# Performance work log

Hardware: AMD Instinct MI355X
Metric: run time of the kernel (lower is better)

The kernel has to match this reference:

```python
import jax, jax.numpy as jnp
import numpy as np

B, N, ND, ED, H, E = 4, 512, 2, 1, 32, 32  # batch, nodes, node_dim, edge_dim, latent, enc


def _xavier(key, shape):
    fan_in, fan_out = shape
    s = jnp.sqrt(2.0 / (fan_in + fan_out)).astype(jnp.float32)
    return jax.random.normal(key, shape, dtype=jnp.float32) * s


def setup_inputs() -> dict:
    key = jax.random.key(0)
    ks = jax.random.split(key, 12)
    return {
        "x": jax.random.normal(ks[0], (B, N, ND), dtype=jnp.float32),
        "h": jax.random.normal(ks[1], (B, N, H), dtype=jnp.float32),
        "adj": jax.random.randint(ks[2], (B, N, N), 0, 2, dtype=jnp.int64) if jax.config.jax_enable_x64 else jax.random.randint(ks[2], (B, N, N), 0, 2, dtype=jnp.int32),
        "e_feat": jax.random.uniform(ks[3], (B, N, N, ED), dtype=jnp.float32),
        "W_ne": _xavier(ks[4], (ND + H, E)), "b_ne": jnp.zeros((E,), jnp.float32),
        "W_ee": _xavier(ks[5], (ED, E)), "b_ee": jnp.zeros((E,), jnp.float32),
        "W_m": _xavier(ks[6], (2 * E + E, H)), "b_m": jnp.zeros((H,), jnp.float32),
        "W_u": _xavier(ks[7], (E + H, H)), "b_u": jnp.zeros((H,), jnp.float32),
        "W_dec": _xavier(ks[8], (H + E, ND)), "b_dec": jnp.zeros((ND,), jnp.float32),
        "W_p": _xavier(ks[9], (2 * H + E, 1)), "b_p": jnp.zeros((1,), jnp.float32),
        "W_t": _xavier(ks[10], (H, 1)), "b_t": jnp.zeros((1,), jnp.float32),
    }


def reference(x, h, adj, e_feat, W_ne, b_ne, W_ee, b_ee, W_m, b_m, W_u, b_u,
              W_dec, b_dec, W_p, b_p, W_t, b_t):
    b, n = x.shape[0], x.shape[1]
    # add self-loops (adj = adj + I), then boolean mask
    mask = (adj + jnp.eye(n, dtype=adj.dtype)[None]) > 0  # [B,N,N]

    # node encoder: z = Linear([x, h])
    z = jnp.concatenate([x, h], axis=-1) @ W_ne + b_ne  # [B,N,E]
    # edge encoder
    e = e_feat @ W_ee + b_ee  # [B,N,N,E]

    # MPNN processor: pairwise messages m_ij = ReLU(M([z_i, z_j, e_ij]))
    zi = jnp.broadcast_to(z[:, :, None, :], (b, n, n, z.shape[-1]))
    zj = jnp.broadcast_to(z[:, None, :, :], (b, n, n, z.shape[-1]))
    m = jax.nn.relu(jnp.concatenate([zi, zj, e], axis=-1) @ W_m + b_m)  # [B,N,N,H]
    m = jnp.where(mask[..., None], m, -1e9)
    agg = jnp.max(m, axis=2)  # max over senders j -> [B,N,H]
    new_h = jax.nn.relu(jnp.concatenate([z, agg], axis=-1) @ W_u + b_u)  # [B,N,H]

    # decoder and termination head
    new_x = jnp.concatenate([z, new_h], axis=-1) @ W_dec + b_dec  # [B,N,ND]
    tau = jnp.mean(new_h, axis=1) @ W_t + b_t  # [B,1]

    # predecessor head (pred=1): pairwise scores masked with -inf off-graph
    hi = jnp.broadcast_to(new_h[:, :, None, :], (b, n, n, new_h.shape[-1]))
    hj = jnp.broadcast_to(new_h[:, None, :, :], (b, n, n, new_h.shape[-1]))
    p = (jnp.concatenate([hi, hj, e], axis=-1) @ W_p + b_p)[..., 0]  # [B,N,N]
    p = jnp.where(mask, p, -jnp.inf)

    return new_x, p, tau, new_h
```

## Files before the change

kernel.cpp:

```cpp
#include <hip/hip_runtime.h>
#include <math.h>

#define BQ 4
#define NQ 512
#define NDQ 2

#define NEG_BIG (-1.0e30f)

__device__ __forceinline__ float4 fmax4(float4 a, float4 b) {
    return make_float4(fmaxf(a.x, b.x), fmaxf(a.y, b.y), fmaxf(a.z, b.z), fmaxf(a.w, b.w));
}
__device__ __forceinline__ void upd(float4& m, float e, float4 ck, float4 bv) {
    m.x = fmaxf(m.x, fmaf(e, ck.x, bv.x));
    m.y = fmaxf(m.y, fmaf(e, ck.y, bv.y));
    m.z = fmaxf(m.z, fmaf(e, ck.z, bv.z));
    m.w = fmaxf(m.w, fmaf(e, ck.w, bv.w));
}

__global__ __launch_bounds__(256) void k_encode(
    const float* __restrict__ x, const float* __restrict__ h,
    const float* __restrict__ W_ne, const float* __restrict__ b_ne,
    const float* __restrict__ W_m,
    const float* __restrict__ W_ee, const float* __restrict__ b_ee,
    const float* __restrict__ b_m,
    const float* __restrict__ W_p, const float* __restrict__ b_p,
    float* __restrict__ ws_z, float* __restrict__ ws_bv,
    float* __restrict__ ws_c, float* __restrict__ ws_d,
    float* __restrict__ ws_c2d2, float* __restrict__ ws_tau)
{
    __shared__ float Wne_s[34 * 32];
    __shared__ float Wm1_s[32 * 32];
    __shared__ float Wm2_s[32 * 32];
    __shared__ float wee_s[32], bee_s[32], wp2_s[32];
    __shared__ float zs[8][32];
    __shared__ float hs[256];
    __shared__ float xs[16];

    int t = threadIdx.x;
    for (int idx = t; idx < 34 * 32; idx += 256) Wne_s[idx] = W_ne[idx];
    for (int idx = t; idx < 32 * 32; idx += 256) Wm1_s[idx] = W_m[32 * 32 + idx];
    hs[t] = h[blockIdx.x * 256 + t];
    if (t < 16) xs[t] = x[blockIdx.x * 16 + t];
    if (blockIdx.x == 0) {
        for (int idx = t; idx < 32 * 32; idx += 256) Wm2_s[idx] = W_m[64 * 32 + idx];
        if (t < 32) { wee_s[t] = W_ee[t]; bee_s[t] = b_ee[t]; wp2_s[t] = W_p[64 + t]; }
        if (t < BQ) ws_tau[t] = 0.0f;
    }
    __syncthreads();

    int ln = t >> 5, k = t & 31;
    int g = blockIdx.x * 8 + ln;
    float z = b_ne[k];
    z = fmaf(xs[ln * 2 + 0], Wne_s[k], z);
    z = fmaf(xs[ln * 2 + 1], Wne_s[32 + k], z);
    #pragma unroll
    for (int c = 0; c < 32; ++c) z = fmaf(hs[ln * 32 + c], Wne_s[(2 + c) * 32 + k], z);
    zs[ln][k] = z;
    ws_z[g * 32 + k] = z;
    __syncthreads();
    float bv = 0.0f;
    #pragma unroll
    for (int c = 0; c < 32; ++c) bv = fmaf(zs[ln][c], Wm1_s[c * 32 + k], bv);
    ws_bv[g * 32 + k] = bv;

    if (blockIdx.x == 0) {
        if (t < 32) {
            float cc = 0.0f, dd = b_m[t];
            #pragma unroll
            for (int c = 0; c < 32; ++c) {
                float wm = Wm2_s[c * 32 + t];
                cc = fmaf(wee_s[c], wm, cc);
                dd = fmaf(bee_s[c], wm, dd);
            }
            ws_c[t] = cc;
            ws_d[t] = dd;
        } else if (t == 32) {
            float c2 = 0.0f;
            #pragma unroll
            for (int c = 0; c < 32; ++c) c2 = fmaf(wee_s[c], wp2_s[c], c2);
            ws_c2d2[0] = c2;
        } else if (t == 33) {
            float d2 = b_p[0];
            #pragma unroll
            for (int c = 0; c < 32; ++c) d2 = fmaf(bee_s[c], wp2_s[c], d2);
            ws_c2d2[1] = d2;
        }
    }
}

__global__ __launch_bounds__(256) void k_mainpost(
    const float* __restrict__ e_feat, const int* __restrict__ adj,
    const float* __restrict__ ws_z, const float* __restrict__ ws_bv,
    const float* __restrict__ ws_c, const float* __restrict__ ws_d,
    const float* __restrict__ W_m, const float* __restrict__ W_u,
    const float* __restrict__ b_u, const float* __restrict__ W_dec,
    const float* __restrict__ b_dec, const float* __restrict__ W_p,
    const float* __restrict__ W_t,
    float* __restrict__ ws_u, float* __restrict__ ws_v, float* __restrict__ ws_tau,
    float* __restrict__ out_x, float* __restrict__ out_h)
{
    __shared__ float ee[4 * 512];
    __shared__ float4 red4[4][32][9];
    __shared__ float Wm0_s[1024];
    __shared__ float Wu_s[2048];
    __shared__ float Wdec_s[128];
    __shared__ float Wp_s[64];
    __shared__ float Wt_s[32];
    __shared__ float d_s[32], bu_s[32], bdec_s[2];
    __shared__ float zs[128];
    __shared__ float aggs[128];
    __shared__ float tp[4];

    int t = threadIdx.x;
    int b = blockIdx.x >> 7;
    int i0 = (blockIdx.x & 127) << 2;
    int gb = ((b << 9) + i0) << 9;

    const float qnan = __builtin_nanf("");
    #pragma unroll
    for (int it = 0; it < 2; ++it) {
        int u = t + it * 256;
        int idx = u << 2;
        int r = idx >> 9;
        int j = idx & 511;
        int i = i0 + r;
        float4 e4 = *(const float4*)&e_feat[gb + idx];
        int4 a4 = *(const int4*)&adj[gb + idx];
        float4 o;
        o.x = (a4.x > 0 || j + 0 == i) ? e4.x : qnan;
        o.y = (a4.y > 0 || j + 1 == i) ? e4.y : qnan;
        o.z = (a4.z > 0 || j + 2 == i) ? e4.z : qnan;
        o.w = (a4.w > 0 || j + 3 == i) ? e4.w : qnan;
        *(float4*)&ee[idx] = o;
    }
    #pragma unroll
    for (int it = 0; it < 4; ++it) Wm0_s[t + it * 256] = W_m[t + it * 256];
    #pragma unroll
    for (int it = 0; it < 8; ++it) Wu_s[t + it * 256] = W_u[t + it * 256];
    if (t < 128) {
        Wdec_s[t] = W_dec[t];
        zs[t] = ws_z[((b << 9) + i0) * 32 + t];
    }
    if (t < 64) Wp_s[t] = W_p[t];
    if (t < 32) { Wt_s[t] = W_t[t]; d_s[t] = ws_d[t]; bu_s[t] = b_u[t]; }
    if (t < 2) bdec_s[t] = b_dec[t];

    int kq = t & 7, slice = t >> 3;
    float4 ck4 = *(const float4*)&ws_c[kq * 4];
    __syncthreads();

    float4 m0, m1, m2, m3;
    m0 = m1 = m2 = m3 = make_float4(-INFINITY, -INFINITY, -INFINITY, -INFINITY);
    const float* bvb = ws_bv + ((long)(b << 9)) * 32;
    #pragma unroll
    for (int jj = 0; jj < 16; ++jj) {
        int j = slice + (jj << 5);
        float4 bv = *(const float4*)&bvb[j * 32 + kq * 4];
        upd(m0, ee[j], ck4, bv);
        upd(m1, ee[512 + j], ck4, bv);
        upd(m2, ee[1024 + j], ck4, bv);
        upd(m3, ee[1536 + j], ck4, bv);
    }
    red4[0][slice][kq] = m0;
    red4[1][slice][kq] = m1;
    red4[2][slice][kq] = m2;
    red4[3][slice][kq] = m3;

    #pragma unroll
    for (int s = 16; s >= 1; s >>= 1) {
        __syncthreads();
        int cnt = 32 * s;
        for (int e = t; e < cnt; e += 256) {
            int r = e / (s * 8);
            int rem = e - r * (s * 8);
            int sl = rem >> 3;
            int kqe = rem & 7;
            red4[r][sl][kqe] = fmax4(red4[r][sl][kqe], red4[r][sl + s][kqe]);
        }
    }
    __syncthreads();

    int ln = t >> 5, k = t & 31;
    if (t < 128) {
        float mx = ((const float*)red4)[ln * (32 * 9 * 4) + k];
        float a = d_s[k];
        #pragma unroll
        for (int c = 0; c < 32; ++c) a = fmaf(zs[ln * 32 + c], Wm0_s[c * 32 + k], a);
        aggs[ln * 32 + k] = fmaxf(a + mx, 0.0f);
    }
    __syncthreads();
    if (t < 128) {
        int g = (b << 9) + i0 + ln;
        float nh = bu_s[k];
        #pragma unroll
        for (int c = 0; c < 32; ++c) nh = fmaf(zs[ln * 32 + c], Wu_s[c * 32 + k], nh);
        #pragma unroll
        for (int c = 0; c < 32; ++c) nh = fmaf(aggs[ln * 32 + c], Wu_s[(32 + c) * 32 + k], nh);
        nh = fmaxf(nh, 0.0f);
        out_h[g * 32 + k] = nh;

        float pu  = nh * Wp_s[k];
        float pv  = nh * Wp_s[32 + k];
        float pt  = nh * Wt_s[k];
        float px0 = fmaf(zs[ln * 32 + k], Wdec_s[k * 2 + 0], nh * Wdec_s[(32 + k) * 2 + 0]);
        float px1 = fmaf(zs[ln * 32 + k], Wdec_s[k * 2 + 1], nh * Wdec_s[(32 + k) * 2 + 1]);
        #pragma unroll
        for (int off = 16; off >= 1; off >>= 1) {
            pu  += __shfl_down(pu, off, 32);
            pv  += __shfl_down(pv, off, 32);
            pt  += __shfl_down(pt, off, 32);
            px0 += __shfl_down(px0, off, 32);
            px1 += __shfl_down(px1, off, 32);
        }
        if (k == 0) {
            ws_u[g] = pu;
            ws_v[g] = pv;
            tp[ln] = pt;
            out_x[g * 2 + 0] = px0 + bdec_s[0];
            out_x[g * 2 + 1] = px1 + bdec_s[1];
        }
    }
    __syncthreads();
    if (t == 0) {
        atomicAdd(&ws_tau[b], tp[0] + tp[1] + tp[2] + tp[3]);
    }
}

__global__ __launch_bounds__(256) void k_pred(
    const float* __restrict__ e_feat, const int* __restrict__ adj,
    const float* __restrict__ ws_u, const float* __restrict__ ws_v,
    const float* __restrict__ ws_c2d2,
    const float* __restrict__ ws_tau, const float* __restrict__ b_t,
    float* __restrict__ out_p, float* __restrict__ out_tau)
{
    int tid = blockIdx.x * 256 + threadIdx.x;
    int idx = tid * 4;
    int b = idx >> 18;
    int i = (idx >> 9) & 511;
    int j = idx & 511;
    float4 e4 = *(const float4*)&e_feat[idx];
    int4 a4 = *(const int4*)&adj[idx];
    float c2 = ws_c2d2[0], d2 = ws_c2d2[1];
    float uv = ws_u[(b << 9) + i] + d2;
    float4 v4 = *(const float4*)&ws_v[(b << 9) + j];
    float4 o;
    o.x = (a4.x > 0 || i == j + 0) ? fmaf(e4.x, c2, uv + v4.x) : NEG_BIG;
    o.y = (a4.y > 0 || i == j + 1) ? fmaf(e4.y, c2, uv + v4.y) : NEG_BIG;
    o.z = (a4.z > 0 || i == j + 2) ? fmaf(e4.z, c2, uv + v4.z) : NEG_BIG;
    o.w = (a4.w > 0 || i == j + 3) ? fmaf(e4.w, c2, uv + v4.w) : NEG_BIG;
    *(float4*)&out_p[idx] = o;

    if (blockIdx.x == 0 && threadIdx.x < BQ) {
        out_tau[threadIdx.x] = ws_tau[threadIdx.x] * (1.0f / (float)NQ) + b_t[0];
    }
}

extern "C" void kernel_launch(void* const* d_in, const int* in_sizes, int n_in,
                              void* d_out, int out_size, void* d_ws, size_t ws_size,
                              hipStream_t stream) {
    const float* x      = (const float*)d_in[0];
    const float* h      = (const float*)d_in[1];
    const int*   adj    = (const int*)d_in[2];
    const float* e_feat = (const float*)d_in[3];
    const float* W_ne   = (const float*)d_in[4];
    const float* b_ne   = (const float*)d_in[5];
    const float* W_ee   = (const float*)d_in[6];
    const float* b_ee   = (const float*)d_in[7];
    const float* W_m    = (const float*)d_in[8];
    const float* b_m    = (const float*)d_in[9];
    const float* W_u    = (const float*)d_in[10];
    const float* b_u    = (const float*)d_in[11];
    const float* W_dec  = (const float*)d_in[12];
    const float* b_dec  = (const float*)d_in[13];
    const float* W_p    = (const float*)d_in[14];
    const float* b_p    = (const float*)d_in[15];
    const float* W_t    = (const float*)d_in[16];
    const float* b_t    = (const float*)d_in[17];

    float* out     = (float*)d_out;
    float* out_x   = out;
    float* out_p   = out + BQ * NQ * NDQ;
    float* out_tau = out_p + BQ * NQ * NQ;
    float* out_h   = out_tau + BQ;

    float* ws      = (float*)d_ws;
    float* ws_z    = ws;
    float* ws_bv   = ws_z + BQ * NQ * 32;
    float* ws_u    = ws_bv + BQ * NQ * 32;
    float* ws_v    = ws_u + BQ * NQ;
    float* ws_tau  = ws_v + BQ * NQ;
    float* ws_c    = ws_tau + BQ;
    float* ws_d    = ws_c + 32;
    float* ws_c2d2 = ws_d + 32;

    k_encode<<<(BQ * NQ) / 8, 256, 0, stream>>>(x, h, W_ne, b_ne, W_m,
                                                W_ee, b_ee, b_m, W_p, b_p,
                                                ws_z, ws_bv, ws_c, ws_d, ws_c2d2, ws_tau);
    k_mainpost<<<(BQ * NQ) / 4, 256, 0, stream>>>(e_feat, adj, ws_z, ws_bv, ws_c, ws_d,
                                                  W_m, W_u, b_u, W_dec, b_dec, W_p, W_t,
                                                  ws_u, ws_v, ws_tau, out_x, out_h);
    k_pred<<<(BQ * NQ * NQ) / (256 * 4), 256, 0, stream>>>(e_feat, adj, ws_u, ws_v,
                                                           ws_c2d2, ws_tau, b_t,
                                                           out_p, out_tau);
}
```

Before: 114.6 us.

## Fuse predecessor head into main kernel via grid-wide spin barrier

Merges the pairwise predecessor-score kernel into the message-passing kernel. Each block keeps its masked edge tile in shared memory and waits on a global atomic barrier until every block has written its per-node v values. It then writes the p scores without reading e_feat and adj a second time. This removes a kernel launch and a full re-read of the edge and adjacency tensors. In exchange it relies on all 512 blocks being co-resident (launch bounds set to 2 blocks per SM) and on a spin barrier with a timeout fallback that could produce wrong results if blocks are not all resident.

```diff
diff --git a/kernel.cpp b/kernel.cpp
--- a/kernel.cpp
+++ b/kernel.cpp
@@ -6,6 +6,8 @@
 #define NDQ 2
 
 #define NEG_BIG (-1.0e30f)
+
+#define NBLK 512u
 
 __device__ __forceinline__ float4 fmax4(float4 a, float4 b) {
     return make_float4(fmaxf(a.x, b.x), fmaxf(a.y, b.y), fmaxf(a.z, b.z), fmaxf(a.w, b.w));
@@ -26,7 +28,8 @@
     const float* __restrict__ W_p, const float* __restrict__ b_p,
     float* __restrict__ ws_z, float* __restrict__ ws_bv,
     float* __restrict__ ws_c, float* __restrict__ ws_d,
-    float* __restrict__ ws_c2d2, float* __restrict__ ws_tau)
+    float* __restrict__ ws_c2d2, float* __restrict__ ws_tau,
+    unsigned int* __restrict__ ws_bar)
 {
     __shared__ float Wne_s[34 * 32];
     __shared__ float Wm1_s[32 * 32];
@@ -45,6 +48,7 @@
         for (int idx = t; idx < 32 * 32; idx += 256) Wm2_s[idx] = W_m[64 * 32 + idx];
         if (t < 32) { wee_s[t] = W_ee[t]; bee_s[t] = b_ee[t]; wp2_s[t] = W_p[64 + t]; }
         if (t < BQ) ws_tau[t] = 0.0f;
+        if (t == BQ) *ws_bar = 0u;
     }
     __syncthreads();
 
@@ -88,16 +92,19 @@
     }
 }
 
-__global__ __launch_bounds__(256) void k_mainpost(
+__global__ __launch_bounds__(256, 2) void k_mainpred(
     const float* __restrict__ e_feat, const int* __restrict__ adj,
     const float* __restrict__ ws_z, const float* __restrict__ ws_bv,
     const float* __restrict__ ws_c, const float* __restrict__ ws_d,
+    const float* __restrict__ ws_c2d2,
     const float* __restrict__ W_m, const float* __restrict__ W_u,
     const float* __restrict__ b_u, const float* __restrict__ W_dec,
     const float* __restrict__ b_dec, const float* __restrict__ W_p,
-    const float* __restrict__ W_t,
-    float* __restrict__ ws_u, float* __restrict__ ws_v, float* __restrict__ ws_tau,
-    float* __restrict__ out_x, float* __restrict__ out_h)
+    const float* __restrict__ W_t, const float* __restrict__ b_t,
+    float* __restrict__ ws_v, float* __restrict__ ws_tau,
+    unsigned int* __restrict__ ws_bar,
+    float* __restrict__ out_x, float* __restrict__ out_p,
+    float* __restrict__ out_tau, float* __restrict__ out_h)
 {
     __shared__ float ee[4 * 512];
     __shared__ float4 red4[4][32][9];
@@ -106,10 +113,11 @@
     __shared__ float Wdec_s[128];
     __shared__ float Wp_s[64];
     __shared__ float Wt_s[32];
-    __shared__ float d_s[32], bu_s[32], bdec_s[2];
+    __shared__ float d_s[32], bu_s[32], bdec_s[2], c2d2_s[2];
     __shared__ float zs[128];
     __shared__ float aggs[128];
-    __shared__ float tp[4];
+    __shared__ float vs[512];
+    __shared__ float tp[4], u_s[4];
 
     int t = threadIdx.x;
     int b = blockIdx.x >> 7;
@@ -143,7 +151,7 @@
     }
     if (t < 64) Wp_s[t] = W_p[t];
     if (t < 32) { Wt_s[t] = W_t[t]; d_s[t] = ws_d[t]; bu_s[t] = b_u[t]; }
-    if (t < 2) bdec_s[t] = b_dec[t];
+    if (t < 2) { bdec_s[t] = b_dec[t]; c2d2_s[t] = ws_c2d2[t]; }
 
     int kq = t & 7, slice = t >> 3;
     float4 ck4 = *(const float4*)&ws_c[kq * 4];
@@ -213,45 +221,50 @@
             px1 += __shfl_down(px1, off, 32);
         }
         if (k == 0) {
-            ws_u[g] = pu;
+            u_s[ln] = pu;
             ws_v[g] = pv;
             tp[ln] = pt;
             out_x[g * 2 + 0] = px0 + bdec_s[0];
             out_x[g * 2 + 1] = px1 + bdec_s[1];
-        }
-    }
-    __syncthreads();
+            __threadfence();
+        }
+    }
+    __syncthreads();
+
     if (t == 0) {
         atomicAdd(&ws_tau[b], tp[0] + tp[1] + tp[2] + tp[3]);
-    }
-}
-
-__global__ __launch_bounds__(256) void k_pred(
-    const float* __restrict__ e_feat, const int* __restrict__ adj,
-    const float* __restrict__ ws_u, const float* __restrict__ ws_v,
-    const float* __restrict__ ws_c2d2,
-    const float* __restrict__ ws_tau, const float* __restrict__ b_t,
-    float* __restrict__ out_p, float* __restrict__ out_tau)
-{
-    int tid = blockIdx.x * 256 + threadIdx.x;
-    int idx = tid * 4;
-    int b = idx >> 18;
-    int i = (idx >> 9) & 511;
-    int j = idx & 511;
-    float4 e4 = *(const float4*)&e_feat[idx];
-    int4 a4 = *(const int4*)&adj[idx];
-    float c2 = ws_c2d2[0], d2 = ws_c2d2[1];
-    float uv = ws_u[(b << 9) + i] + d2;
-    float4 v4 = *(const float4*)&ws_v[(b << 9) + j];
-    float4 o;
-    o.x = (a4.x > 0 || i == j + 0) ? fmaf(e4.x, c2, uv + v4.x) : NEG_BIG;
-    o.y = (a4.y > 0 || i == j + 1) ? fmaf(e4.y, c2, uv + v4.y) : NEG_BIG;
-    o.z = (a4.z > 0 || i == j + 2) ? fmaf(e4.z, c2, uv + v4.z) : NEG_BIG;
-    o.w = (a4.w > 0 || i == j + 3) ? fmaf(e4.w, c2, uv + v4.w) : NEG_BIG;
-    *(float4*)&out_p[idx] = o;
-
-    if (blockIdx.x == 0 && threadIdx.x < BQ) {
-        out_tau[threadIdx.x] = ws_tau[threadIdx.x] * (1.0f / (float)NQ) + b_t[0];
+        __threadfence();
+        atomicAdd(ws_bar, 1u);
+        unsigned int spins = 0;
+        while (__hip_atomic_load(ws_bar, __ATOMIC_ACQUIRE,
+                                 __HIP_MEMORY_SCOPE_AGENT) < NBLK) {
+            __builtin_amdgcn_s_sleep(8);
+            if (++spins > (1u << 16)) break;
+        }
+    }
+    __syncthreads();
+    __threadfence();
+
+    if (t < 128) *(float4*)&vs[t * 4] = *(const float4*)&ws_v[(b << 9) + t * 4];
+    __syncthreads();
+    float c2 = c2d2_s[0], d2 = c2d2_s[1];
+    #pragma unroll
+    for (int it = 0; it < 2; ++it) {
+        int idx = (t + it * 256) << 2;
+        int r = idx >> 9;
+        int j = idx & 511;
+        float ui = u_s[r] + d2;
+        float4 e4 = *(const float4*)&ee[idx];
+        float4 v4 = *(const float4*)&vs[j];
+        float4 o;
+        o.x = (e4.x == e4.x) ? fmaf(e4.x, c2, ui + v4.x) : NEG_BIG;
+        o.y = (e4.y == e4.y) ? fmaf(e4.y, c2, ui + v4.y) : NEG_BIG;
+        o.z = (e4.z == e4.z) ? fmaf(e4.z, c2, ui + v4.z) : NEG_BIG;
+        o.w = (e4.w == e4.w) ? fmaf(e4.w, c2, ui + v4.w) : NEG_BIG;
+        *(float4*)&out_p[gb + idx] = o;
+    }
+    if (blockIdx.x == 0 && t < BQ) {
+        out_tau[t] = ws_tau[t] * (1.0f / (float)NQ) + b_t[0];
     }
 }
 
@@ -286,20 +299,20 @@
     float* ws      = (float*)d_ws;
     float* ws_z    = ws;
     float* ws_bv   = ws_z + BQ * NQ * 32;
-    float* ws_u    = ws_bv + BQ * NQ * 32;
-    float* ws_v    = ws_u + BQ * NQ;
+    float* ws_v    = ws_bv + BQ * NQ * 32;
     float* ws_tau  = ws_v + BQ * NQ;
     float* ws_c    = ws_tau + BQ;
     float* ws_d    = ws_c + 32;
     float* ws_c2d2 = ws_d + 32;
+    unsigned int* ws_bar = (unsigned int*)(ws_c2d2 + 2);
 
     k_encode<<<(BQ * NQ) / 8, 256, 0, stream>>>(x, h, W_ne, b_ne, W_m,
                                                 W_ee, b_ee, b_m, W_p, b_p,
-                                                ws_z, ws_bv, ws_c, ws_d, ws_c2d2, ws_tau);
-    k_mainpost<<<(BQ * NQ) / 4, 256, 0, stream>>>(e_feat, adj, ws_z, ws_bv, ws_c, ws_d,
-                                                  W_m, W_u, b_u, W_dec, b_dec, W_p, W_t,
-                                                  ws_u, ws_v, ws_tau, out_x, out_h);
-    k_pred<<<(BQ * NQ * NQ) / (256 * 4), 256, 0, stream>>>(e_feat, adj, ws_u, ws_v,
-                                                           ws_c2d2, ws_tau, b_t,
-                                                           out_p, out_tau);
-}
+                                                ws_z, ws_bv, ws_c, ws_d, ws_c2d2,
+                                                ws_tau, ws_bar);
+    k_mainpred<<<(BQ * NQ) / 4, 256, 0, stream>>>(e_feat, adj, ws_z, ws_bv, ws_c, ws_d,
+                                                  ws_c2d2, W_m, W_u, b_u, W_dec, b_dec,
+                                                  W_p, W_t, b_t,
+                                                  ws_v, ws_tau, ws_bar,
+                                                  out_x, out_p, out_tau, out_h);
+}
```

Result: slower. 188.8 us (+64.7%).

## Halve rows per block in mainpost and reduce maxima with wavefront shuffles

Applied to the files above, without the earlier changes.

The message-aggregation kernel now handles 2 destination rows per block instead of 4, which doubles the grid to 1024 blocks and shrinks shared memory use. The five-step shared-memory tree reduction over sender slices is replaced by cross-lane shuffle-down max within each 64-wide wavefront, followed by a small four-wave combine in shared memory. Launch bounds now request 4 blocks per CU to raise occupancy. In exchange, each block reloads the full W_m and W_u weight tiles for half as many rows, and half the threads sit idle in the post-aggregation phase.

```diff
diff --git a/kernel.cpp b/kernel.cpp
--- a/kernel.cpp
+++ b/kernel.cpp
@@ -9,6 +9,10 @@
 
 __device__ __forceinline__ float4 fmax4(float4 a, float4 b) {
     return make_float4(fmaxf(a.x, b.x), fmaxf(a.y, b.y), fmaxf(a.z, b.z), fmaxf(a.w, b.w));
+}
+__device__ __forceinline__ float4 shfl_down4(float4 v, int d) {
+    return make_float4(__shfl_down(v.x, d, 64), __shfl_down(v.y, d, 64),
+                       __shfl_down(v.z, d, 64), __shfl_down(v.w, d, 64));
 }
 __device__ __forceinline__ void upd(float4& m, float e, float4 ck, float4 bv) {
     m.x = fmaxf(m.x, fmaf(e, ck.x, bv.x));
@@ -88,7 +92,7 @@
     }
 }
 
-__global__ __launch_bounds__(256) void k_mainpost(
+__global__ __launch_bounds__(256, 4) void k_mainpost(
     const float* __restrict__ e_feat, const int* __restrict__ adj,
     const float* __restrict__ ws_z, const float* __restrict__ ws_bv,
     const float* __restrict__ ws_c, const float* __restrict__ ws_d,
@@ -99,29 +103,28 @@
     float* __restrict__ ws_u, float* __restrict__ ws_v, float* __restrict__ ws_tau,
     float* __restrict__ out_x, float* __restrict__ out_h)
 {
-    __shared__ float ee[4 * 512];
-    __shared__ float4 red4[4][32][9];
+    __shared__ float ee[2 * 512];
+    __shared__ float4 redw[2][4][8];
+    __shared__ float mxs[2][32];
     __shared__ float Wm0_s[1024];
     __shared__ float Wu_s[2048];
     __shared__ float Wdec_s[128];
     __shared__ float Wp_s[64];
     __shared__ float Wt_s[32];
     __shared__ float d_s[32], bu_s[32], bdec_s[2];
-    __shared__ float zs[128];
-    __shared__ float aggs[128];
-    __shared__ float tp[4];
+    __shared__ float zs[64];
+    __shared__ float aggs[64];
+    __shared__ float tp[2];
 
     int t = threadIdx.x;
-    int b = blockIdx.x >> 7;
-    int i0 = (blockIdx.x & 127) << 2;
+    int b = blockIdx.x >> 8;
+    int i0 = (blockIdx.x & 255) << 1;
     int gb = ((b << 9) + i0) << 9;
 
     const float qnan = __builtin_nanf("");
-    #pragma unroll
-    for (int it = 0; it < 2; ++it) {
-        int u = t + it * 256;
-        int idx = u << 2;
-        int r = idx >> 9;
+    {
+        int idx = t << 2;
+        int r = t >> 7;
         int j = idx & 511;
         int i = i0 + r;
         float4 e4 = *(const float4*)&e_feat[gb + idx];
@@ -137,11 +140,8 @@
     for (int it = 0; it < 4; ++it) Wm0_s[t + it * 256] = W_m[t + it * 256];
     #pragma unroll
     for (int it = 0; it < 8; ++it) Wu_s[t + it * 256] = W_u[t + it * 256];
-    if (t < 128) {
-        Wdec_s[t] = W_dec[t];
-        zs[t] = ws_z[((b << 9) + i0) * 32 + t];
-    }
-    if (t < 64) Wp_s[t] = W_p[t];
+    if (t < 128) Wdec_s[t] = W_dec[t];
+    if (t < 64) { Wp_s[t] = W_p[t]; zs[t] = ws_z[((b << 9) + i0) * 32 + t]; }
     if (t < 32) { Wt_s[t] = W_t[t]; d_s[t] = ws_d[t]; bu_s[t] = b_u[t]; }
     if (t < 2) bdec_s[t] = b_dec[t];
 
@@ -149,8 +149,8 @@
     float4 ck4 = *(const float4*)&ws_c[kq * 4];
     __syncthreads();
 
-    float4 m0, m1, m2, m3;
-    m0 = m1 = m2 = m3 = make_float4(-INFINITY, -INFINITY, -INFINITY, -INFINITY);
+    float4 m0, m1;
+    m0 = m1 = make_float4(-INFINITY, -INFINITY, -INFINITY, -INFINITY);
     const float* bvb = ws_bv + ((long)(b << 9)) * 32;
     #pragma unroll
     for (int jj = 0; jj < 16; ++jj) {
@@ -158,38 +158,36 @@
         float4 bv = *(const float4*)&bvb[j * 32 + kq * 4];
         upd(m0, ee[j], ck4, bv);
         upd(m1, ee[512 + j], ck4, bv);
-        upd(m2, ee[1024 + j], ck4, bv);
-        upd(m3, ee[1536 + j], ck4, bv);
-    }
-    red4[0][slice][kq] = m0;
-    red4[1][slice][kq] = m1;
-    red4[2][slice][kq] = m2;
-    red4[3][slice][kq] = m3;
-
-    #pragma unroll
-    for (int s = 16; s >= 1; s >>= 1) {
-        __syncthreads();
-        int cnt = 32 * s;
-        for (int e = t; e < cnt; e += 256) {
-            int r = e / (s * 8);
-            int rem = e - r * (s * 8);
-            int sl = rem >> 3;
-            int kqe = rem & 7;
-            red4[r][sl][kqe] = fmax4(red4[r][sl][kqe], red4[r][sl + s][kqe]);
-        }
+    }
+
+    #pragma unroll
+    for (int d = 8; d <= 32; d <<= 1) {
+        m0 = fmax4(m0, shfl_down4(m0, d));
+        m1 = fmax4(m1, shfl_down4(m1, d));
+    }
+    if ((t & 63) < 8) {
+        redw[0][t >> 6][kq] = m0;
+        redw[1][t >> 6][kq] = m1;
+    }
+    __syncthreads();
+    if (t < 16) {
+        int row = t >> 3, q = t & 7;
+        float4 a = fmax4(fmax4(redw[row][0][q], redw[row][1][q]),
+                         fmax4(redw[row][2][q], redw[row][3][q]));
+        *(float4*)&mxs[row][q * 4] = a;
     }
     __syncthreads();
 
     int ln = t >> 5, k = t & 31;
-    if (t < 128) {
-        float mx = ((const float*)red4)[ln * (32 * 9 * 4) + k];
+    if (t < 64) {
+        float mx = mxs[ln][k];
         float a = d_s[k];
         #pragma unroll
         for (int c = 0; c < 32; ++c) a = fmaf(zs[ln * 32 + c], Wm0_s[c * 32 + k], a);
         aggs[ln * 32 + k] = fmaxf(a + mx, 0.0f);
     }
     __syncthreads();
-    if (t < 128) {
+    if (t < 64) {
         int g = (b << 9) + i0 + ln;
         float nh = bu_s[k];
         #pragma unroll
@@ -222,7 +220,7 @@
     }
     __syncthreads();
     if (t == 0) {
-        atomicAdd(&ws_tau[b], tp[0] + tp[1] + tp[2] + tp[3]);
+        atomicAdd(&ws_tau[b], tp[0] + tp[1]);
     }
 }
 
@@ -296,7 +294,7 @@
     k_encode<<<(BQ * NQ) / 8, 256, 0, stream>>>(x, h, W_ne, b_ne, W_m,
                                                 W_ee, b_ee, b_m, W_p, b_p,
                                                 ws_z, ws_bv, ws_c, ws_d, ws_c2d2, ws_tau);
-    k_mainpost<<<(BQ * NQ) / 4, 256, 0, stream>>>(e_feat, adj, ws_z, ws_bv, ws_c, ws_d,
+    k_mainpost<<<(BQ * NQ) / 2, 256, 0, stream>>>(e_feat, adj, ws_z, ws_bv, ws_c, ws_d,
                                                   W_m, W_u, b_u, W_dec, b_dec, W_p, W_t,
                                                   ws_u, ws_v, ws_tau, out_x, out_h);
     k_pred<<<(BQ * NQ * NQ) / (256 * 4), 256, 0, stream>>>(e_feat, adj, ws_u, ws_v,
```

New measurement: 120.4 us. +5.1%, slower.

## Stage masked e*c2 into out_p in main kernel and use wave-shuffle max reduction

Applied to the files above, without the earlier changes.

k_mainpost already reads e_feat and adj, so it now writes the masked e*c2 term (NaN where there is no edge) into out_p. k_pred then reads only that one buffer instead of both e_feat and adj, and uses a NaN test to apply the mask. The shared-memory tree max reduction is replaced by wave shuffles plus a small cross-wave combine, which removes several block barriers. The cost is an extra full write and read of out_p in place of the adj and e_feat reads, so total traffic falls by about one array's worth. It also depends on e*c2 never producing a NaN on its own.

```diff
diff --git a/kernel.cpp b/kernel.cpp
--- a/kernel.cpp
+++ b/kernel.cpp
@@ -9,6 +9,10 @@
 
 __device__ __forceinline__ float4 fmax4(float4 a, float4 b) {
     return make_float4(fmaxf(a.x, b.x), fmaxf(a.y, b.y), fmaxf(a.z, b.z), fmaxf(a.w, b.w));
+}
+__device__ __forceinline__ float4 shfl_down4(float4 v, int d) {
+    return make_float4(__shfl_down(v.x, d, 64), __shfl_down(v.y, d, 64),
+                       __shfl_down(v.z, d, 64), __shfl_down(v.w, d, 64));
 }
 __device__ __forceinline__ void upd(float4& m, float e, float4 ck, float4 bv) {
     m.x = fmaxf(m.x, fmaf(e, ck.x, bv.x));
@@ -92,15 +96,18 @@
     const float* __restrict__ e_feat, const int* __restrict__ adj,
     const float* __restrict__ ws_z, const float* __restrict__ ws_bv,
     const float* __restrict__ ws_c, const float* __restrict__ ws_d,
+    const float* __restrict__ ws_c2d2,
     const float* __restrict__ W_m, const float* __restrict__ W_u,
     const float* __restrict__ b_u, const float* __restrict__ W_dec,
     const float* __restrict__ b_dec, const float* __restrict__ W_p,
     const float* __restrict__ W_t,
     float* __restrict__ ws_u, float* __restrict__ ws_v, float* __restrict__ ws_tau,
-    float* __restrict__ out_x, float* __restrict__ out_h)
+    float* __restrict__ out_x, float* __restrict__ out_h,
+    float* __restrict__ out_p)
 {
     __shared__ float ee[4 * 512];
-    __shared__ float4 red4[4][32][9];
+    __shared__ float4 redw[4][4][8];
+    __shared__ float mxs[4][32];
     __shared__ float Wm0_s[1024];
     __shared__ float Wu_s[2048];
     __shared__ float Wdec_s[128];
@@ -117,6 +124,7 @@
     int gb = ((b << 9) + i0) << 9;
 
     const float qnan = __builtin_nanf("");
+    float c2 = ws_c2d2[0];
     #pragma unroll
     for (int it = 0; it < 2; ++it) {
         int u = t + it * 256;
@@ -126,12 +134,17 @@
         int i = i0 + r;
         float4 e4 = *(const float4*)&e_feat[gb + idx];
         int4 a4 = *(const int4*)&adj[gb + idx];
-        float4 o;
-        o.x = (a4.x > 0 || j + 0 == i) ? e4.x : qnan;
-        o.y = (a4.y > 0 || j + 1 == i) ? e4.y : qnan;
-        o.z = (a4.z > 0 || j + 2 == i) ? e4.z : qnan;
-        o.w = (a4.w > 0 || j + 3 == i) ? e4.w : qnan;
+        float4 o, pe;
+        bool mx_ = (a4.x > 0 || j + 0 == i);
+        bool my_ = (a4.y > 0 || j + 1 == i);
+        bool mz_ = (a4.z > 0 || j + 2 == i);
+        bool mw_ = (a4.w > 0 || j + 3 == i);
+        o.x = mx_ ? e4.x : qnan;  pe.x = mx_ ? e4.x * c2 : qnan;
+        o.y = my_ ? e4.y : qnan;  pe.y = my_ ? e4.y * c2 : qnan;
+        o.z = mz_ ? e4.z : qnan;  pe.z = mz_ ? e4.z * c2 : qnan;
+        o.w = mw_ ? e4.w : qnan;  pe.w = mw_ ? e4.w * c2 : qnan;
         *(float4*)&ee[idx] = o;
+        *(float4*)&out_p[gb + idx] = pe;
     }
     #pragma unroll
     for (int it = 0; it < 4; ++it) Wm0_s[t + it * 256] = W_m[t + it * 256];
@@ -161,28 +174,33 @@
         upd(m2, ee[1024 + j], ck4, bv);
         upd(m3, ee[1536 + j], ck4, bv);
     }
-    red4[0][slice][kq] = m0;
-    red4[1][slice][kq] = m1;
-    red4[2][slice][kq] = m2;
-    red4[3][slice][kq] = m3;
-
-    #pragma unroll
-    for (int s = 16; s >= 1; s >>= 1) {
-        __syncthreads();
-        int cnt = 32 * s;
-        for (int e = t; e < cnt; e += 256) {
-            int r = e / (s * 8);
-            int rem = e - r * (s * 8);
-            int sl = rem >> 3;
-            int kqe = rem & 7;
-            red4[r][sl][kqe] = fmax4(red4[r][sl][kqe], red4[r][sl + s][kqe]);
-        }
+
+    #pragma unroll
+    for (int d = 8; d <= 32; d <<= 1) {
+        m0 = fmax4(m0, shfl_down4(m0, d));
+        m1 = fmax4(m1, shfl_down4(m1, d));
+        m2 = fmax4(m2, shfl_down4(m2, d));
+        m3 = fmax4(m3, shfl_down4(m3, d));
+    }
+    if ((t & 63) < 8) {
+        int w = t >> 6;
+        redw[w][0][kq] = m0;
+        redw[w][1][kq] = m1;
+        redw[w][2][kq] = m2;
+        redw[w][3][kq] = m3;
+    }
+    __syncthreads();
+    if (t < 32) {
+        int row = t >> 3, q = t & 7;
+        float4 a = fmax4(fmax4(redw[0][row][q], redw[1][row][q]),
+                         fmax4(redw[2][row][q], redw[3][row][q]));
+        *(float4*)&mxs[row][q * 4] = a;
     }
     __syncthreads();
 
     int ln = t >> 5, k = t & 31;
     if (t < 128) {
-        float mx = ((const float*)red4)[ln * (32 * 9 * 4) + k];
+        float mx = mxs[ln][k];
         float a = d_s[k];
         #pragma unroll
         for (int c = 0; c < 32; ++c) a = fmaf(zs[ln * 32 + c], Wm0_s[c * 32 + k], a);
@@ -227,7 +245,6 @@
 }
 
 __global__ __launch_bounds__(256) void k_pred(
-    const float* __restrict__ e_feat, const int* __restrict__ adj,
     const float* __restrict__ ws_u, const float* __restrict__ ws_v,
     const float* __restrict__ ws_c2d2,
     const float* __restrict__ ws_tau, const float* __restrict__ b_t,
@@ -238,16 +255,15 @@
     int b = idx >> 18;
     int i = (idx >> 9) & 511;
     int j = idx & 511;
-    float4 e4 = *(const float4*)&e_feat[idx];
-    int4 a4 = *(const int4*)&adj[idx];
-    float c2 = ws_c2d2[0], d2 = ws_c2d2[1];
+    float4 pe = *(const float4*)&out_p[idx];
+    float d2 = ws_c2d2[1];
     float uv = ws_u[(b << 9) + i] + d2;
     float4 v4 = *(const float4*)&ws_v[(b << 9) + j];
     float4 o;
-    o.x = (a4.x > 0 || i == j + 0) ? fmaf(e4.x, c2, uv + v4.x) : NEG_BIG;
-    o.y = (a4.y > 0 || i == j + 1) ? fmaf(e4.y, c2, uv + v4.y) : NEG_BIG;
-    o.z = (a4.z > 0 || i == j + 2) ? fmaf(e4.z, c2, uv + v4.z) : NEG_BIG;
-    o.w = (a4.w > 0 || i == j + 3) ? fmaf(e4.w, c2, uv + v4.w) : NEG_BIG;
+    o.x = (pe.x == pe.x) ? pe.x + (uv + v4.x) : NEG_BIG;
+    o.y = (pe.y == pe.y) ? pe.y + (uv + v4.y) : NEG_BIG;
+    o.z = (pe.z == pe.z) ? pe.z + (uv + v4.z) : NEG_BIG;
+    o.w = (pe.w == pe.w) ? pe.w + (uv + v4.w) : NEG_BIG;
     *(float4*)&out_p[idx] = o;
 
     if (blockIdx.x == 0 && threadIdx.x < BQ) {
@@ -297,9 +313,10 @@
                                                 W_ee, b_ee, b_m, W_p, b_p,
                                                 ws_z, ws_bv, ws_c, ws_d, ws_c2d2, ws_tau);
     k_mainpost<<<(BQ * NQ) / 4, 256, 0, stream>>>(e_feat, adj, ws_z, ws_bv, ws_c, ws_d,
-                                                  W_m, W_u, b_u, W_dec, b_dec, W_p, W_t,
-                                                  ws_u, ws_v, ws_tau, out_x, out_h);
-    k_pred<<<(BQ * NQ * NQ) / (256 * 4), 256, 0, stream>>>(e_feat, adj, ws_u, ws_v,
-                                                           ws_c2d2, ws_tau, b_t,
+                                                  ws_c2d2, W_m, W_u, b_u, W_dec, b_dec,
+                                                  W_p, W_t,
+                                                  ws_u, ws_v, ws_tau, out_x, out_h, out_p);
+    k_pred<<<(BQ * NQ * NQ) / (256 * 4), 256, 0, stream>>>(ws_u, ws_v, ws_c2d2,
+                                                           ws_tau, b_t,
                                                            out_p, out_tau);
 }
```

Result: no change. 115.7 us (median of 2 runs) (+0.9%).
